# Optimization experiments

Measured on AMD Instinct MI355X. Metric: run time of the kernel, lower is better.

Reference implementation:

```python
import jax, jax.numpy as jnp
import numpy as np

N_NODES = 100000
N_EDGES = 1600000
D = 128
LEAKY_ALPHA = 0.2
ELU_ALPHA = 1.0


def setup_inputs() -> dict:
    key = jax.random.key(0)
    ks = jax.random.split(key, 8)
    s = 0.05
    atom_features = jax.random.normal(ks[0], (N_NODES, D), dtype=jnp.float32)
    W1 = jax.random.normal(ks[1], (1, 2 * D), dtype=jnp.float32) * s
    b1 = jnp.zeros((1,), dtype=jnp.float32)
    W2 = jax.random.normal(ks[2], (D, D), dtype=jnp.float32) * s
    b2 = jnp.zeros((D,), dtype=jnp.float32)
    w_ih = jax.random.normal(ks[3], (3 * D, D), dtype=jnp.float32) * s
    w_hh = jax.random.normal(ks[4], (3 * D, D), dtype=jnp.float32) * s
    b_ih = jnp.zeros((3 * D,), dtype=jnp.float32)
    b_hh = jnp.zeros((3 * D,), dtype=jnp.float32)
    edge_index = jax.random.randint(ks[5], (2, N_EDGES), 0, N_NODES, dtype=jnp.int64)
    return {"atom_features": atom_features, "W1": W1, "b1": b1, "W2": W2,
            "b2": b2, "w_ih": w_ih, "w_hh": w_hh, "b_ih": b_ih, "b_hh": b_hh,
            "edge_index": edge_index}


def _elu(x, alpha):
    return jnp.where(x > 0, x, alpha * (jnp.exp(jnp.minimum(x, 0.0)) - 1.0))


def reference(atom_features, W1, b1, W2, b2, w_ih, w_hh, b_ih, b_hh, edge_index):
    N, d = atom_features.shape
    src = edge_index[0]  # neighbor j (keys[0])
    dst = edge_index[1]  # center node i (keys[1])

    # atom_fc2 transform (dropout is identity in eval)
    nft = atom_features @ W2.T + b2  # [N, d]

    # attention logit per edge: leaky_relu(W1 @ concat(h_dst, h_src) + b1)
    w_d = W1[0, :d]
    w_s = W1[0, d:]
    logit = atom_features @ w_d  # [N]
    logit_src = atom_features @ w_s  # [N]
    score = logit[dst] + logit_src[src] + b1[0]  # [E]
    score = jnp.where(score > 0, score, LEAKY_ALPHA * score)

    # segment softmax over incoming edges of each dst node
    m = jax.ops.segment_max(score, dst, num_segments=N)  # -inf for isolated nodes
    m_safe = jnp.where(jnp.isfinite(m), m, 0.0)
    e = jnp.exp(score - m_safe[dst])  # [E]
    denom = jax.ops.segment_sum(e, dst, num_segments=N)  # [N]
    attn = e / denom[dst]  # [E]

    # weighted scatter-sum of transformed neighbor features
    msg = attn[:, None] * nft[src]  # [E, d]
    transform = jax.ops.segment_sum(msg, dst, num_segments=N)  # [N, d]
    context = _elu(transform, ELU_ALPHA)

    deg = jax.ops.segment_sum(jnp.ones_like(score), dst, num_segments=N)
    out_emb = jnp.where(deg[:, None] > 0, context, atom_features)

    # GRUCell(out_emb, atom_features): torch gate ordering r, z, n
    gi = out_emb @ w_ih.T + b_ih  # [N, 3d]
    gh = atom_features @ w_hh.T + b_hh  # [N, 3d]
    gi_r, gi_z, gi_n = jnp.split(gi, 3, axis=-1)
    gh_r, gh_z, gh_n = jnp.split(gh, 3, axis=-1)
    r = jax.nn.sigmoid(gi_r + gh_r)
    z = jax.nn.sigmoid(gi_z + gh_z)
    n = jnp.tanh(gi_n + r * gh_n)
    h_new = (1.0 - z) * n + z * atom_features
    return h_new
```

## Files before the change

kernel.cpp:

```cpp
#include <hip/hip_runtime.h>
#include <cstdint>
#include <cstddef>

#define D 128
#define LEAKY_ALPHA 0.2f

#define BSHIFT 8
#define BCAP 4608
#define NBUK_MAX 512

typedef __attribute__((ext_vector_type(8))) short short8;
typedef __attribute__((ext_vector_type(4))) short short4v;
typedef __attribute__((ext_vector_type(4))) float f32x4;
typedef __attribute__((ext_vector_type(2))) float f32x2;

static __device__ __forceinline__ unsigned short f32_to_bf16_rne(float v) {
  unsigned x = __float_as_uint(v);
  unsigned r = (x + 0x7fffu + ((x >> 16) & 1u)) >> 16;
  return (unsigned short)r;
}
static __device__ __forceinline__ float bf16_to_f32(unsigned short u) {
  return __uint_as_float(((unsigned)u) << 16);
}

#if __has_builtin(__builtin_amdgcn_cvt_pk_f32_fp8) && __has_builtin(__builtin_amdgcn_cvt_pk_fp8_f32)
#define FP8_HW 1
#endif

static __device__ __forceinline__ unsigned char f32_to_fp8(float x) {
#ifdef FP8_HW
  return (unsigned char)(__builtin_amdgcn_cvt_pk_fp8_f32(x, x, 0, false) & 0xff);
#else
  unsigned u = __float_as_uint(x);
  unsigned s = (u >> 24) & 0x80u;
  unsigned mag = u & 0x7fffffffu;
  if (mag == 0) return (unsigned char)s;
  int e = (int)(mag >> 23) - 127;
  unsigned full = (mag & 0x7fffffu) | 0x800000u;
  if (e >= 9) return (unsigned char)(s | 0x7Eu);
  int sh = (e >= -6) ? 20 : 20 + (-6 - e);
  if (sh > 24) return (unsigned char)s;
  unsigned keep = full >> sh;
  unsigned rem = full & ((1u << sh) - 1u);
  unsigned half = 1u << (sh - 1);
  if (rem > half || (rem == half && (keep & 1u))) keep++;
  unsigned em;
  if (e >= -6) {
    unsigned v = ((unsigned)(e + 7) << 3) + keep - 8u;
    if (v > 0x7Eu) v = 0x7Eu;
    em = v;
  } else {
    em = keep;
  }
  return (unsigned char)(s | em);
#endif
}

#ifndef FP8_HW
static __device__ __forceinline__ float fp8_dec(unsigned b) {
  unsigned em = b & 0x7fu, s = (b & 0x80u) << 24;
  float m;
  if (em >= 8) m = __uint_as_float(0x3C000000u + (em << 20));
  else m = (float)em * 0.001953125f;
  return __uint_as_float(s | __float_as_uint(m));
}
#endif

static __device__ __forceinline__ void fp8_fma16(uint4 u, float e, float* acc) {
#ifdef FP8_HW
  f32x2 t;
  t = __builtin_amdgcn_cvt_pk_f32_fp8(u.x, false); acc[0] += e*t[0]; acc[1] += e*t[1];
  t = __builtin_amdgcn_cvt_pk_f32_fp8(u.x, true ); acc[2] += e*t[0]; acc[3] += e*t[1];
  t = __builtin_amdgcn_cvt_pk_f32_fp8(u.y, false); acc[4] += e*t[0]; acc[5] += e*t[1];
  t = __builtin_amdgcn_cvt_pk_f32_fp8(u.y, true ); acc[6] += e*t[0]; acc[7] += e*t[1];
  t = __builtin_amdgcn_cvt_pk_f32_fp8(u.z, false); acc[8] += e*t[0]; acc[9] += e*t[1];
  t = __builtin_amdgcn_cvt_pk_f32_fp8(u.z, true ); acc[10]+= e*t[0]; acc[11]+= e*t[1];
  t = __builtin_amdgcn_cvt_pk_f32_fp8(u.w, false); acc[12]+= e*t[0]; acc[13]+= e*t[1];
  t = __builtin_amdgcn_cvt_pk_f32_fp8(u.w, true ); acc[14]+= e*t[0]; acc[15]+= e*t[1];
#else
  unsigned ws[4] = {u.x, u.y, u.z, u.w};
  #pragma unroll
  for (int k = 0; k < 4; ++k)
    #pragma unroll
    for (int b = 0; b < 4; ++b)
      acc[k * 4 + b] += e * fp8_dec((ws[k] >> (8 * b)) & 0xffu);
#endif
}

__global__ __launch_bounds__(256) void k_wprep(
    const float* __restrict__ W1, const float* __restrict__ W2,
    const float* __restrict__ w_ih, const float* __restrict__ w_hh,
    unsigned short* __restrict__ Wcat, unsigned short* __restrict__ Wb) {
  int idx = blockIdx.x * 256 + threadIdx.x;
  if (idx < 144 * 128) {
    int r = idx >> 7, c = idx & 127;
    float v = 0.f;
    if (r < 128)      v = W2[r * 128 + c];
    else if (r == 128) v = W1[c];
    else if (r == 129) v = W1[128 + c];
    Wcat[idx] = f32_to_bf16_rne(v);
    return;
  }
  int i2 = idx - 144 * 128;
  if (i2 < 384 * 256) {
    int r = i2 >> 8, c = i2 & 255;
    float v = (c < D) ? w_ih[r * D + c] : w_hh[r * D + (c - D)];
    Wb[i2] = f32_to_bf16_rne(v);
  }
}

#define NPITCH 136
__global__ __launch_bounds__(256, 2) void k_nft_mfma(
    const float* __restrict__ A, const unsigned short* __restrict__ Wcat,
    const float* __restrict__ b2, unsigned char* __restrict__ nftb,
    float* __restrict__ logit_d, float* __restrict__ logit_s,
    unsigned short* __restrict__ X, int N) {
  __shared__ short sA[64 * NPITCH];
  int tid = threadIdx.x;
  int n0 = blockIdx.x * 64;

  #pragma unroll
  for (int i = 0; i < 8; ++i) {
    int g = i * 1024 + tid * 4;
    int row = g >> 7, col = g & 127;
    int gr = n0 + row; if (gr >= N) gr = N - 1;
    float4 v = *(const float4*)&A[(size_t)gr * D + col];
    short4v b;
    b.x = (short)f32_to_bf16_rne(v.x);
    b.y = (short)f32_to_bf16_rne(v.y);
    b.z = (short)f32_to_bf16_rne(v.z);
    b.w = (short)f32_to_bf16_rne(v.w);
    *(short4v*)&sA[row * NPITCH + col] = b;
  }
  __syncthreads();

  int w = tid >> 6, lane = tid & 63, l15 = lane & 15, l4 = lane >> 4;

  f32x4 acc[4][2], acc8[4];
  #pragma unroll
  for (int rt = 0; rt < 4; ++rt) {
    acc[rt][0] = (f32x4)0.f; acc[rt][1] = (f32x4)0.f; acc8[rt] = (f32x4)0.f;
  }

  #pragma unroll
  for (int ks = 0; ks < 4; ++ks) {
    int kk = ks * 32 + l4 * 8;
    short8 a[4];
    #pragma unroll
    for (int rt = 0; rt < 4; ++rt)
      a[rt] = *(const short8*)&sA[(rt * 16 + l15) * NPITCH + kk];
    short8 b0 = *(const short8*)&Wcat[(size_t)(w * 16 + l15) * 128 + kk];
    short8 b1 = *(const short8*)&Wcat[(size_t)((w + 4) * 16 + l15) * 128 + kk];
    #pragma unroll
    for (int rt = 0; rt < 4; ++rt) {
      acc[rt][0] = __builtin_amdgcn_mfma_f32_16x16x32_bf16(a[rt], b0, acc[rt][0], 0, 0, 0);
      acc[rt][1] = __builtin_amdgcn_mfma_f32_16x16x32_bf16(a[rt], b1, acc[rt][1], 0, 0, 0);
    }
    if (w == 0) {
      short8 b2v = *(const short8*)&Wcat[(size_t)(128 + l15) * 128 + kk];
      #pragma unroll
      for (int rt = 0; rt < 4; ++rt)
        acc8[rt] = __builtin_amdgcn_mfma_f32_16x16x32_bf16(a[rt], b2v, acc8[rt], 0, 0, 0);
    }
  }

  #pragma unroll
  for (int i = 0; i < 4; ++i) {
    int g = i * 2048 + tid * 8;
    int row = g >> 7, col = g & 127;
    if (n0 + row < N) {
      short8 v = *(const short8*)&sA[row * NPITCH + col];
      *(short8*)&X[(size_t)(n0 + row) * 256 + 128 + col] = v;
    }
  }

  #pragma unroll
  for (int t = 0; t < 2; ++t) {
    int j = (w + 4 * t) * 16 + l15;
    float bb = b2[j];
    #pragma unroll
    for (int rt = 0; rt < 4; ++rt)
      #pragma unroll
      for (int jr = 0; jr < 4; ++jr) {
        int row = n0 + rt * 16 + l4 * 4 + jr;
        if (row < N)
          nftb[(size_t)row * D + j] = f32_to_fp8(acc[rt][t][jr] + bb);
      }
  }
  if (w == 0 && l15 < 2) {
    float* dst = (l15 == 0) ? logit_d : logit_s;
    #pragma unroll
    for (int rt = 0; rt < 4; ++rt)
      #pragma unroll
      for (int jr = 0; jr < 4; ++jr) {
        int row = n0 + rt * 16 + l4 * 4 + jr;
        if (row < N) dst[row] = acc8[rt][jr];
      }
  }
}

__global__ __launch_bounds__(256) void k_part(
    const int* __restrict__ ei, unsigned* __restrict__ cursors,
    unsigned* __restrict__ part, int E, int NBUK, int EPB) {
  __shared__ int hist[NBUK_MAX];
  __shared__ int sbase[NBUK_MAX];
  int t = threadIdx.x;
  int e0 = blockIdx.x * EPB;
  int e1 = min(e0 + EPB, E);
  for (int i = t; i < NBUK; i += 256) hist[i] = 0;
  __syncthreads();
  for (int e = e0 + t; e < e1; e += 256)
    atomicAdd(&hist[ei[E + e] >> BSHIFT], 1);
  __syncthreads();
  for (int i = t; i < NBUK; i += 256) {
    int h = hist[i];
    sbase[i] = h ? (int)atomicAdd(&cursors[i * 16], (unsigned)h) : 0;
    hist[i] = 0;
  }
  __syncthreads();
  for (int e = e0 + t; e < e1; e += 256) {
    int src = ei[e];
    int dst = ei[E + e];
    int b = dst >> BSHIFT;
    int lp = sbase[b] + atomicAdd(&hist[b], 1);
    if (lp < BCAP)
      part[(size_t)b * BCAP + lp] =
          ((unsigned)(dst & ((1 << BSHIFT) - 1)) << 24) | (unsigned)src;
  }
}

__global__ __launch_bounds__(256) void k_bucket_csr(
    const unsigned* __restrict__ cursors, unsigned* __restrict__ part,
    int2* __restrict__ beg_end, int N) {
  __shared__ unsigned ents[BCAP];
  __shared__ int hist[256];
  __shared__ int scn[256];
  __shared__ int cur[256];
  int b = blockIdx.x, t = threadIdx.x;
  int nb0 = b << BSHIFT;
  int cnt = (int)cursors[b * 16];
  if (cnt > BCAP) cnt = BCAP;
  hist[t] = 0;
  __syncthreads();
  unsigned* reg = part + (size_t)b * BCAP;
  for (int i = t; i < cnt; i += 256) {
    unsigned p = reg[i];
    ents[i] = p;
    atomicAdd(&hist[p >> 24], 1);
  }
  __syncthreads();
  int v = hist[t];
  scn[t] = v;
  __syncthreads();
  for (int o = 1; o < 256; o <<= 1) {
    int x = (t >= o) ? scn[t - o] : 0;
    __syncthreads();
    scn[t] += x;
    __syncthreads();
  }
  int excl = scn[t] - v;
  cur[t] = excl;
  int n = nb0 + t;
  if (n < N) beg_end[n] = make_int2(b * BCAP + excl, b * BCAP + excl + v);
  __syncthreads();
  for (int i = t; i < cnt; i += 256) {
    unsigned p = ents[i];
    int lp = atomicAdd(&cur[p >> 24], 1);
    reg[lp] = p & 0xFFFFFFu;
  }
}

#define XPITCH 264
__global__ __launch_bounds__(512, 2) void k_gat_gru(
    const int2* __restrict__ beg_end, const unsigned* __restrict__ srcs,
    const float* __restrict__ logit_d, const float* __restrict__ logit_s,
    const float* __restrict__ b1, const unsigned char* __restrict__ nftb,
    const unsigned short* X,
    const unsigned short* __restrict__ Wb,
    const float* __restrict__ b_ih, const float* __restrict__ b_hh,
    float* out, int N) {
  __shared__ short sX[64 * XPITCH];
  int tid = threadIdx.x;
  int n0 = blockIdx.x * 64;

  #pragma unroll
  for (int i = 0; i < 2; ++i) {
    int idx = i * 512 + tid;
    int row = idx >> 4, c8 = idx & 15;
    int gr = n0 + row; if (gr >= N) gr = N - 1;
    short8 v = *(const short8*)&X[(size_t)gr * 256 + 128 + c8 * 8];
    *(short8*)&sX[row * XPITCH + 128 + c8 * 8] = v;
  }
  __syncthreads();

  {
    int l  = tid & 7;
    int nl = tid >> 3;
    int n  = n0 + nl;
    short8 xo0, xo1;
    if (n < N) {
      int2 be = beg_end[n];
      int start = be.x, end = be.y;
      if (end == start) {
        xo0 = *(const short8*)&sX[nl * XPITCH + 128 + l * 16];
        xo1 = *(const short8*)&sX[nl * XPITCH + 128 + l * 16 + 8];
      } else {
        float ld = logit_d[n] + b1[0];
        float acc[16];
        #pragma unroll
        for (int j = 0; j < 16; ++j) acc[j] = 0.f;
        float den = 0.f;
        int p = start;
        for (; p + 2 <= end; p += 2) {
          int s0 = (int)srcs[p], s1 = (int)srcs[p + 1];
          float ls0 = logit_s[s0], ls1 = logit_s[s1];
          uint4 u0 = *(const uint4*)&nftb[(size_t)s0 * D + l * 16];
          uint4 u1 = *(const uint4*)&nftb[(size_t)s1 * D + l * 16];
          float t0 = ld + ls0; t0 = t0 > 0.f ? t0 : LEAKY_ALPHA * t0;
          float t1 = ld + ls1; t1 = t1 > 0.f ? t1 : LEAKY_ALPHA * t1;
          float e0 = __expf(t0), e1 = __expf(t1);
          den += e0 + e1;
          fp8_fma16(u0, e0, acc);
          fp8_fma16(u1, e1, acc);
        }
        if (p < end) {
          int s0 = (int)srcs[p];
          float t0 = ld + logit_s[s0]; t0 = t0 > 0.f ? t0 : LEAKY_ALPHA * t0;
          float e0 = __expf(t0);
          uint4 u0 = *(const uint4*)&nftb[(size_t)s0 * D + l * 16];
          den += e0;
          fp8_fma16(u0, e0, acc);
        }
        float inv = 1.f / den;
        #pragma unroll
        for (int j = 0; j < 16; ++j) {
          float t = acc[j] * inv;
          float oe = t > 0.f ? t : (__expf(t) - 1.f);
          if (j < 8) xo0[j] = (short)f32_to_bf16_rne(oe);
          else       xo1[j - 8] = (short)f32_to_bf16_rne(oe);
        }
      }
    } else {
      xo0 = (short8)0; xo1 = (short8)0;
    }
    *(short8*)&sX[nl * XPITCH + l * 16]     = xo0;
    *(short8*)&sX[nl * XPITCH + l * 16 + 8] = xo1;
  }
  __syncthreads();

  int w    = tid >> 6;
  int lane = tid & 63;
  int l15  = lane & 15;
  int l4   = lane >> 4;
  int j    = w * 16 + l15;

  f32x4 acc[4][4];
  #pragma unroll
  for (int rt = 0; rt < 4; ++rt)
    #pragma unroll
    for (int q = 0; q < 4; ++q) acc[rt][q] = (f32x4)0.f;

  #pragma unroll
  for (int ks = 0; ks < 8; ++ks) {
    int kk = ks * 32 + l4 * 8;
    short8 a[4];
    #pragma unroll
    for (int rt = 0; rt < 4; ++rt)
      a[rt] = *(const short8*)&sX[(rt * 16 + l15) * XPITCH + kk];
    short8 b0 = *(const short8*)&Wb[(size_t)(j) * 256 + kk];
    short8 b1 = *(const short8*)&Wb[(size_t)(128 + j) * 256 + kk];
    short8 b2 = *(const short8*)&Wb[(size_t)(256 + j) * 256 + kk];
    int qn = (ks < 4) ? 2 : 3;
    #pragma unroll
    for (int rt = 0; rt < 4; ++rt) {
      acc[rt][0]  = __builtin_amdgcn_mfma_f32_16x16x32_bf16(a[rt], b0, acc[rt][0], 0, 0, 0);
      acc[rt][1]  = __builtin_amdgcn_mfma_f32_16x16x32_bf16(a[rt], b1, acc[rt][1], 0, 0, 0);
      acc[rt][qn] = __builtin_amdgcn_mfma_f32_16x16x32_bf16(a[rt], b2, acc[rt][qn], 0, 0, 0);
    }
  }

  float br  = b_ih[j] + b_hh[j];
  float bz  = b_ih[D + j] + b_hh[D + j];
  float bin = b_ih[2 * D + j];
  float bhn = b_hh[2 * D + j];
  #pragma unroll
  for (int rt = 0; rt < 4; ++rt) {
    #pragma unroll
    for (int jr = 0; jr < 4; ++jr) {
      int lrow = rt * 16 + l4 * 4 + jr;
      int row = n0 + lrow;
      if (row < N) {
        float rp  = acc[rt][0][jr] + br;
        float zp  = acc[rt][1][jr] + bz;
        float gin = acc[rt][2][jr] + bin;
        float ghn = acc[rt][3][jr] + bhn;
        float r = 1.f / (1.f + __expf(-rp));
        float z = 1.f / (1.f + __expf(-zp));
        float t = gin + r * ghn;
        float e2 = __expf(2.f * t);
        float nn = 1.f - 2.f / (e2 + 1.f);
        float h = bf16_to_f32((unsigned short)sX[lrow * XPITCH + 128 + j]);
        out[(size_t)row * D + j] = (1.f - z) * nn + z * h;
      }
    }
  }
}

extern "C" void kernel_launch(void* const* d_in, const int* in_sizes, int n_in,
                              void* d_out, int out_size, void* d_ws, size_t ws_size,
                              hipStream_t stream) {
  const float* A    = (const float*)d_in[0];
  const float* W1   = (const float*)d_in[1];
  const float* b1   = (const float*)d_in[2];
  const float* W2   = (const float*)d_in[3];
  const float* b2   = (const float*)d_in[4];
  const float* w_ih = (const float*)d_in[5];
  const float* w_hh = (const float*)d_in[6];
  const float* b_ih = (const float*)d_in[7];
  const float* b_hh = (const float*)d_in[8];
  const int*   ei   = (const int*)d_in[9];

  int N = in_sizes[0] / D;
  int E = in_sizes[9] / 2;
  float* out = (float*)d_out;

  int NBUK = (N + (1 << BSHIFT) - 1) >> BSHIFT;

  char* ws = (char*)d_ws;
  unsigned char* nftb = (unsigned char*)ws;
  float* logit_d = (float*)(ws + (size_t)N * D);
  float* logit_s = logit_d + N;
  int2*  beg_end = (int2*)(logit_s + N);
  unsigned* cursors = (unsigned*)(beg_end + N);
  unsigned* part = cursors + (size_t)NBUK * 16;
  unsigned short* Wb   = (unsigned short*)(part + (size_t)NBUK * BCAP);
  unsigned short* Wcat = Wb + 384 * 256;

  hipMemsetAsync(cursors, 0, (size_t)NBUK * 16 * sizeof(unsigned), stream);

  k_wprep<<<(144 * 128 + 384 * 256 + 255) / 256, 256, 0, stream>>>(
      W1, W2, w_ih, w_hh, Wcat, Wb);
  k_nft_mfma<<<(N + 63) / 64, 256, 0, stream>>>(A, Wcat, b2, nftb,
                                                logit_d, logit_s,
                                                (unsigned short*)d_out, N);
  int gridPart = 160;
  int EPB = (E + gridPart - 1) / gridPart;
  k_part<<<gridPart, 256, 0, stream>>>(ei, cursors, part, E, NBUK, EPB);
  k_bucket_csr<<<NBUK, 256, 0, stream>>>(cursors, part, beg_end, N);
  k_gat_gru<<<(N + 63) / 64, 512, 0, stream>>>(beg_end, part, logit_d, logit_s,
                                               b1, nftb,
                                               (const unsigned short*)d_out,
                                               Wb, b_ih, b_hh, out, N);
}
```

Baseline: 201.8 us.

## Pre-gather source logits into CSR edge records and unroll aggregation by four

Result: no change. 199.3 us (-1.3%).

```diff
diff --git a/kernel.cpp b/kernel.cpp
--- a/kernel.cpp
+++ b/kernel.cpp
@@ -230,7 +230,8 @@
 }
 
 __global__ __launch_bounds__(256) void k_bucket_csr(
-    const unsigned* __restrict__ cursors, unsigned* __restrict__ part,
+    const unsigned* __restrict__ cursors, const unsigned* __restrict__ part,
+    const float* __restrict__ logit_s, uint2* __restrict__ rec,
     int2* __restrict__ beg_end, int N) {
   __shared__ unsigned ents[BCAP];
   __shared__ int hist[256];
@@ -242,7 +243,8 @@
   if (cnt > BCAP) cnt = BCAP;
   hist[t] = 0;
   __syncthreads();
-  unsigned* reg = part + (size_t)b * BCAP;
+  const unsigned* reg = part + (size_t)b * BCAP;
+  uint2* rrec = rec + (size_t)b * BCAP;
   for (int i = t; i < cnt; i += 256) {
     unsigned p = reg[i];
     ents[i] = p;
@@ -266,15 +268,16 @@
   for (int i = t; i < cnt; i += 256) {
     unsigned p = ents[i];
     int lp = atomicAdd(&cur[p >> 24], 1);
-    reg[lp] = p & 0xFFFFFFu;
+    unsigned s = p & 0xFFFFFFu;
+    rrec[lp] = make_uint2(s, __float_as_uint(logit_s[s]));
   }
 }
 
 #define XPITCH 264
-__global__ __launch_bounds__(512, 2) void k_gat_gru(
-    const int2* __restrict__ beg_end, const unsigned* __restrict__ srcs,
-    const float* __restrict__ logit_d, const float* __restrict__ logit_s,
-    const float* __restrict__ b1, const unsigned char* __restrict__ nftb,
+__global__ __launch_bounds__(512, 1) void k_gat_gru(
+    const int2* __restrict__ beg_end, const uint2* __restrict__ rec,
+    const float* __restrict__ logit_d, const float* __restrict__ b1,
+    const unsigned char* __restrict__ nftb,
     const unsigned short* X,
     const unsigned short* __restrict__ Wb,
     const float* __restrict__ b_ih, const float* __restrict__ b_hh,
@@ -311,25 +314,30 @@
         for (int j = 0; j < 16; ++j) acc[j] = 0.f;
         float den = 0.f;
         int p = start;
-        for (; p + 2 <= end; p += 2) {
-          int s0 = (int)srcs[p], s1 = (int)srcs[p + 1];
-          float ls0 = logit_s[s0], ls1 = logit_s[s1];
-          uint4 u0 = *(const uint4*)&nftb[(size_t)s0 * D + l * 16];
-          uint4 u1 = *(const uint4*)&nftb[(size_t)s1 * D + l * 16];
-          float t0 = ld + ls0; t0 = t0 > 0.f ? t0 : LEAKY_ALPHA * t0;
-          float t1 = ld + ls1; t1 = t1 > 0.f ? t1 : LEAKY_ALPHA * t1;
-          float e0 = __expf(t0), e1 = __expf(t1);
-          den += e0 + e1;
+        for (; p + 4 <= end; p += 4) {
+          uint2 r0 = rec[p], r1 = rec[p + 1], r2 = rec[p + 2], r3 = rec[p + 3];
+          uint4 u0 = *(const uint4*)&nftb[(size_t)r0.x * D + l * 16];
+          uint4 u1 = *(const uint4*)&nftb[(size_t)r1.x * D + l * 16];
+          uint4 u2 = *(const uint4*)&nftb[(size_t)r2.x * D + l * 16];
+          uint4 u3 = *(const uint4*)&nftb[(size_t)r3.x * D + l * 16];
+          float t0 = ld + __uint_as_float(r0.y); t0 = t0 > 0.f ? t0 : LEAKY_ALPHA * t0;
+          float t1 = ld + __uint_as_float(r1.y); t1 = t1 > 0.f ? t1 : LEAKY_ALPHA * t1;
+          float t2 = ld + __uint_as_float(r2.y); t2 = t2 > 0.f ? t2 : LEAKY_ALPHA * t2;
+          float t3 = ld + __uint_as_float(r3.y); t3 = t3 > 0.f ? t3 : LEAKY_ALPHA * t3;
+          float e0 = __expf(t0), e1 = __expf(t1), e2 = __expf(t2), e3 = __expf(t3);
+          den += (e0 + e1) + (e2 + e3);
           fp8_fma16(u0, e0, acc);
           fp8_fma16(u1, e1, acc);
+          fp8_fma16(u2, e2, acc);
+          fp8_fma16(u3, e3, acc);
         }
-        if (p < end) {
-          int s0 = (int)srcs[p];
-          float t0 = ld + logit_s[s0]; t0 = t0 > 0.f ? t0 : LEAKY_ALPHA * t0;
+        for (; p < end; ++p) {
+          uint2 r = rec[p];
+          uint4 u = *(const uint4*)&nftb[(size_t)r.x * D + l * 16];
+          float t0 = ld + __uint_as_float(r.y); t0 = t0 > 0.f ? t0 : LEAKY_ALPHA * t0;
           float e0 = __expf(t0);
-          uint4 u0 = *(const uint4*)&nftb[(size_t)s0 * D + l * 16];
           den += e0;
-          fp8_fma16(u0, e0, acc);
+          fp8_fma16(u, e0, acc);
         }
         float inv = 1.f / den;
         #pragma unroll
@@ -433,7 +441,8 @@
   int2*  beg_end = (int2*)(logit_s + N);
   unsigned* cursors = (unsigned*)(beg_end + N);
   unsigned* part = cursors + (size_t)NBUK * 16;
-  unsigned short* Wb   = (unsigned short*)(part + (size_t)NBUK * BCAP);
+  uint2* rec = (uint2*)(part + (size_t)NBUK * BCAP);
+  unsigned short* Wb   = (unsigned short*)(rec + (size_t)NBUK * BCAP);
   unsigned short* Wcat = Wb + 384 * 256;
 
   hipMemsetAsync(cursors, 0, (size_t)NBUK * 16 * sizeof(unsigned), stream);
@@ -446,9 +455,9 @@
   int gridPart = 160;
   int EPB = (E + gridPart - 1) / gridPart;
   k_part<<<gridPart, 256, 0, stream>>>(ei, cursors, part, E, NBUK, EPB);
-  k_bucket_csr<<<NBUK, 256, 0, stream>>>(cursors, part, beg_end, N);
-  k_gat_gru<<<(N + 63) / 64, 512, 0, stream>>>(beg_end, part, logit_d, logit_s,
-                                               b1, nftb,
+  k_bucket_csr<<<NBUK, 256, 0, stream>>>(cursors, part, logit_s, rec,
+                                         beg_end, N);
+  k_gat_gru<<<(N + 63) / 64, 512, 0, stream>>>(beg_end, rec, logit_d, b1, nftb,
                                                (const unsigned short*)d_out,
                                                Wb, b_ih, b_hh, out, N);
 }
```
